# Kernel optimization log

Hardware: AMD Instinct MI355X
Metric: run time of the kernel (lower is better)

Reference implementation:

```python
import jax, jax.numpy as jnp
import numpy as np

D_MODEL = 256; N_HEADS = 8; N_LEVELS = 4; N_POINTS = 4
D_HEAD = D_MODEL // N_HEADS


def setup_inputs() -> dict:
    key = jax.random.key(0)
    ks = jax.random.split(key, 8)
    N, Lq = 4, 4096
    shapes = np.array([4096, 2048, 1024, 512], dtype=np.int32)  # temporal lengths per level
    Len_in = int(shapes.sum())  # 7680
    start = np.concatenate([[0], np.cumsum(shapes)[:-1]]).astype(np.int32)
    HLP = N_HEADS * N_LEVELS * N_POINTS
    return {
        "query": jax.random.normal(ks[0], (N, Lq, D_MODEL), jnp.float32),
        "reference_points": jax.random.uniform(ks[1], (N, Lq, N_LEVELS, 1), jnp.float32),
        "input_flatten": jax.random.normal(ks[2], (N, Len_in, D_MODEL), jnp.float32),
        "input_spatial_shapes": jnp.asarray(shapes),
        "input_level_start_index": jnp.asarray(start),
        "W_off": jax.random.normal(ks[3], (D_MODEL, HLP), jnp.float32) * 0.01,
        "b_off": jax.random.normal(ks[4], (HLP,), jnp.float32) * 2.0,
        "W_aw": jax.random.normal(ks[5], (D_MODEL, HLP), jnp.float32) * 0.02,
        "b_aw": jnp.zeros((HLP,), jnp.float32),
        "W_v": jax.random.normal(ks[6], (D_MODEL, D_MODEL), jnp.float32) / np.sqrt(D_MODEL).astype(np.float32),
        "b_v": jnp.zeros((D_MODEL,), jnp.float32),
        "W_out": jax.random.normal(ks[7], (D_MODEL, D_MODEL), jnp.float32) / np.sqrt(D_MODEL).astype(np.float32),
        "b_out": jnp.zeros((D_MODEL,), jnp.float32),
    }


def reference(query, reference_points, input_flatten, input_spatial_shapes,
              input_level_start_index, W_off, b_off, W_aw, b_aw, W_v, b_v,
              W_out, b_out):
    N, Lq, C = query.shape
    M, L, P, Dh = N_HEADS, N_LEVELS, N_POINTS, D_HEAD
    S = input_flatten.shape[1]

    value = (input_flatten @ W_v + b_v).reshape(N, S, M, Dh)
    off = (query @ W_off + b_off).reshape(N, Lq, M, L, P)
    aw = jax.nn.softmax((query @ W_aw + b_aw).reshape(N, Lq, M, L * P), axis=-1)
    aw = aw.reshape(N, Lq, M, L, P)

    # reference_points last dim == 1 branch: loc = ref + off / T_l, in [0,1]
    T = input_spatial_shapes.astype(jnp.float32)[None, None, None, :, None]  # [1,1,1,L,1]
    loc = reference_points[:, :, None, :, None, 0] + off / T  # [N,Lq,M,L,P]

    # grid_sample(align_corners=False, padding_mode='border') along W with H=1, y=0.5:
    # pixel coord x = loc*T - 0.5, clamped to [0, T-1], then linear interp.
    x = jnp.clip(loc * T - 0.5, 0.0, T - 1.0)
    x0 = jnp.floor(x)
    w1 = x - x0                                   # frac weight for right neighbor
    i0 = x0.astype(jnp.int32)
    i1 = jnp.minimum(i0 + 1, input_spatial_shapes[None, None, None, :, None] - 1)
    base = input_level_start_index[None, None, None, :, None]
    g0 = i0 + base                                # global flattened indices [N,Lq,M,L,P]
    g1 = i1 + base

    v = value.transpose(0, 2, 1, 3)               # [N,M,S,Dh]

    def gather(idx):
        idxt = idx.transpose(0, 2, 1, 3, 4).reshape(N, M, Lq * L * P, 1)
        return jnp.take_along_axis(v, idxt, axis=2).reshape(N, M, Lq, L, P, Dh)

    s0 = gather(g0)
    s1 = gather(g1)
    w1t = w1.transpose(0, 2, 1, 3, 4)[..., None]   # [N,M,Lq,L,P,1]
    samp = s0 * (1.0 - w1t) + s1 * w1t             # [N,M,Lq,L,P,Dh]

    awt = aw.transpose(0, 2, 1, 3, 4)[..., None]
    out = (samp * awt).sum(axis=(3, 4))            # [N,M,Lq,Dh]
    out = out.transpose(0, 2, 1, 3).reshape(N, Lq, M * Dh)
    return out @ W_out + b_out
```

## Files before the change

kernel.cpp:

```cpp
#include <hip/hip_runtime.h>
#include <hip/hip_bf16.h>
#include <cstddef>
#include <cstdint>

#define D_MODEL   256
#define N_HEADS   8
#define N_LEVELS  4
#define N_POINTS  4
#define D_HEAD    32
#define HLP       128
#define NBATCH    4
#define LQ        4096
#define S_LEN     7680

typedef __attribute__((ext_vector_type(8))) short  short8;
typedef __attribute__((ext_vector_type(4))) float  f32x4;
typedef __attribute__((ext_vector_type(4))) int    i32x4;
typedef __attribute__((ext_vector_type(8))) unsigned short ushort8;

__device__ __forceinline__ unsigned short f2bf(float x) {
    __hip_bfloat16 h = __float2bfloat16(x);
    return *reinterpret_cast<unsigned short*>(&h);
}
__device__ __forceinline__ float bf2f(unsigned short u) {
    unsigned int v = ((unsigned int)u) << 16;
    return *reinterpret_cast<float*>(&v);
}

__device__ __forceinline__ void gload_lds16(const void* g, void* l) {
    __builtin_amdgcn_global_load_lds(
        (const __attribute__((address_space(1))) void*)g,
        (__attribute__((address_space(3))) void*)l,
        16, 0, 0);
}

__global__ __launch_bounds__(256) void prep_kernel(
    const float* __restrict__ W_v,  const float* __restrict__ W_off,
    const float* __restrict__ W_aw, const float* __restrict__ W_out,
    const float* __restrict__ b_off, const float* __restrict__ b_aw,
    unsigned short* __restrict__ Wv_t, unsigned short* __restrict__ Wcat_t,
    unsigned short* __restrict__ Wout_t, float* __restrict__ bcat)
{
    __shared__ float t[64][65];
    const int z   = blockIdx.z;
    const int k0  = blockIdx.y * 64;
    const int n0  = blockIdx.x * 64;
    const int tid = threadIdx.x;

    const float* src; int srcN; int cs; unsigned short* dst;
    if (z == 0)      { src = W_v;   srcN = 256; cs = n0;       dst = Wv_t;  }
    else if (z == 2) { src = W_out; srcN = 256; cs = n0;       dst = Wout_t;}
    else if (n0 < 128){ src = W_off; srcN = 128; cs = n0;      dst = Wcat_t;}
    else             { src = W_aw;  srcN = 128; cs = n0 - 128; dst = Wcat_t;}

    #pragma unroll
    for (int i = 0; i < 16; ++i) {
        int idx = tid + i * 256;
        int kk = idx >> 6, nn = idx & 63;
        t[kk][nn] = src[(size_t)(k0 + kk) * srcN + cs + nn];
    }
    __syncthreads();
    #pragma unroll
    for (int i = 0; i < 16; ++i) {
        int idx = tid + i * 256;
        int nn = idx >> 6, kk = idx & 63;
        dst[(size_t)(n0 + nn) * 256 + k0 + kk] = f2bf(t[kk][nn]);
    }
    if (z == 1 && blockIdx.x == 0 && blockIdx.y == 0) {
        bcat[tid] = (tid < 128) ? b_off[tid] : b_aw[tid - 128];
    }
}

__global__ __launch_bounds__(256) void gemm_vp_kernel(
    const float* __restrict__ inflat, const float* __restrict__ query,
    const unsigned short* __restrict__ Wv_t, const unsigned short* __restrict__ Wcat_t,
    const float* __restrict__ b_v, const float* __restrict__ bcat,
    unsigned short* __restrict__ value3, float* __restrict__ P)
{
    __shared__ alignas(16) unsigned short Abuf[2][4][64][8];
    __shared__ alignas(16) unsigned short Bbuf[2][8][64][8];

    const int job = blockIdx.x;
    const bool is_val = (job < 960);
    const int jj   = is_val ? job : (job - 960);
    const int row0 = (jj >> 1) * 64;
    const int col0 = (jj & 1) * 128;
    const float* A = is_val ? inflat : query;
    const unsigned short* Bt = is_val ? Wv_t : Wcat_t;
    const float* bias = is_val ? b_v : bcat;

    const int tid  = threadIdx.x;
    const int lane = tid & 63;
    const int w    = tid >> 6;
    const int lr   = lane & 15;
    const int lk   = (lane >> 4) * 8;

    const int ar = tid >> 2;
    const int ak = (tid & 3) * 8;
    const int afrag = ar >> 4;
    const int alane = ((ak >> 3) << 4) | (ar & 15);
    const float* Arow = A + (size_t)(row0 + ar) * 256 + ak;
    const unsigned short* Bcol = Bt + (size_t)(col0 + lr) * 256 + lk;

    f32x4 acc[8] = {};

    float4 pa0 = *(const float4*)(Arow);
    float4 pa1 = *(const float4*)(Arow + 4);
    #pragma unroll
    for (int c = 0; c < 2; ++c) {
        const int in = w * 2 + c;
        gload_lds16(Bcol + (size_t)in * 16 * 256, &Bbuf[0][in][0][0]);
    }

    for (int kt = 0; kt < 8; ++kt) {
        const int cur = kt & 1;
        short8 pk;
        pk[0] = (short)f2bf(pa0.x); pk[1] = (short)f2bf(pa0.y);
        pk[2] = (short)f2bf(pa0.z); pk[3] = (short)f2bf(pa0.w);
        pk[4] = (short)f2bf(pa1.x); pk[5] = (short)f2bf(pa1.y);
        pk[6] = (short)f2bf(pa1.z); pk[7] = (short)f2bf(pa1.w);
        *(short8*)&Abuf[cur][afrag][alane][0] = pk;
        __syncthreads();

        if (kt < 7) {
            const int k1 = (kt + 1) * 32;
            pa0 = *(const float4*)(Arow + k1);
            pa1 = *(const float4*)(Arow + k1 + 4);
            #pragma unroll
            for (int c = 0; c < 2; ++c) {
                const int in = w * 2 + c;
                gload_lds16(Bcol + (size_t)in * 16 * 256 + k1, &Bbuf[1 - cur][in][0][0]);
            }
        }

        const short8 af = *(const short8*)&Abuf[cur][w][lane][0];
        #pragma unroll
        for (int j = 0; j < 8; ++j) {
            const short8 bf = *(const short8*)&Bbuf[cur][j][lane][0];
            acc[j] = __builtin_amdgcn_mfma_f32_16x16x32_bf16(af, bf, acc[j], 0, 0, 0);
        }
    }

    const int prow = (lane >> 4) * 4;
    const int pcol = lane & 15;
    const int rbase = row0 + w * 16 + prow;
    if (is_val) {
        const int n  = row0 / S_LEN;
        const int s0 = row0 - n * S_LEN + w * 16 + prow;
        #pragma unroll
        for (int j = 0; j < 8; ++j) {
            const int col = col0 + j * 16 + pcol;
            const float bs = bias[col];
            const int m = col >> 5, d = col & 31;
            unsigned short* dst = value3 + ((size_t)(n * 8 + m) * S_LEN + s0) * 32 + d;
            #pragma unroll
            for (int r = 0; r < 4; ++r)
                dst[(size_t)r * 32] = f2bf(acc[j][r] + bs);
        }
    } else {
        #pragma unroll
        for (int j = 0; j < 8; ++j) {
            const int col = col0 + j * 16 + pcol;
            const float bs = bias[col];
            #pragma unroll
            for (int r = 0; r < 4; ++r)
                P[(size_t)(rbase + r) * 256 + col] = acc[j][r] + bs;
        }
    }
}

__global__ __launch_bounds__(256) void sample_out_kernel(
    const float* __restrict__ P, const float* __restrict__ refp,
    const int* __restrict__ shapes, const int* __restrict__ lstart,
    const unsigned short* __restrict__ value3,
    const unsigned short* __restrict__ Wout_t,
    const float* __restrict__ b_out,
    float* __restrict__ Cout)
{
    __shared__ int   sG0[16][132];
    __shared__ float sW [16][132];
    __shared__ float sA [16][132];
    __shared__ alignas(16) unsigned short t_lds[16][264];
    __shared__ int   glim[4];

    const int b    = blockIdx.x;
    const int xcd  = b & 7;
    const int n    = xcd >> 1;
    const int half = xcd & 1;
    const int slot = b >> 3;
    const int q0   = (slot * 2 + half) * 16;
    const int nq0  = n * LQ + q0;
    const int tid  = threadIdx.x;

    if (tid < 4) glim[tid] = lstart[tid] + shapes[tid] - 1;

    #pragma unroll
    for (int it = 0; it < 2; ++it) {
        const int idx = tid + it * 256;
        const int q   = idx >> 5;
        const int sub = idx & 31;
        const int m   = sub >> 2;
        const int l   = sub & 3;
        const int j0  = m * 16 + l * 4;
        const int nq  = nq0 + q;
        const f32x4 off   = __builtin_nontemporal_load(
            (const f32x4*)(P + (size_t)nq * 256 + j0));
        const f32x4 logit = __builtin_nontemporal_load(
            (const f32x4*)(P + (size_t)nq * 256 + 128 + j0));
        const float ref   = refp[(size_t)nq * N_LEVELS + l];
        const int   sh    = shapes[l];
        const int   ls    = lstart[l];
        const float Tf    = (float)sh;
        i32x4 g4; f32x4 w4;
        #pragma unroll
        for (int k = 0; k < 4; ++k) {
            float x = ref * Tf + off[k] - 0.5f;
            x = fminf(fmaxf(x, 0.0f), Tf - 1.0f);
            const float x0 = floorf(x);
            g4[k] = (int)x0 + ls;
            w4[k] = x - x0;
        }
        *(i32x4*)&sG0[q][j0] = g4;
        *(f32x4*)&sW [q][j0] = w4;
        *(f32x4*)&sA [q][j0] = logit;
    }
    __syncthreads();

    #pragma unroll
    for (int it = 0; it < 2; ++it) {
        const int idx = tid + it * 256;
        const int q   = idx >> 5;
        const int sub = idx & 31;
        const int m   = sub >> 2;
        const int ql  = sub & 3;
        const unsigned short* vb =
            value3 + (size_t)(n * 8 + m) * S_LEN * 32 + ql * 8;

        float e[16];
        {
            const f32x4 a0 = *(const f32x4*)&sA[q][m * 16 + 0];
            const f32x4 a1 = *(const f32x4*)&sA[q][m * 16 + 4];
            const f32x4 a2 = *(const f32x4*)&sA[q][m * 16 + 8];
            const f32x4 a3 = *(const f32x4*)&sA[q][m * 16 + 12];
            #pragma unroll
            for (int k = 0; k < 4; ++k) {
                e[k] = a0[k]; e[4+k] = a1[k]; e[8+k] = a2[k]; e[12+k] = a3[k];
            }
        }
        float mx = -1e30f;
        #pragma unroll
        for (int i = 0; i < 16; ++i) mx = fmaxf(mx, e[i]);
        float s = 0.f;
        #pragma unroll
        for (int i = 0; i < 16; ++i) { e[i] = __expf(e[i] - mx); s += e[i]; }
        const float rs = 1.0f / s;

        float acc[8] = {};
        #pragma unroll
        for (int i = 0; i < 16; ++i) {
            const int j = m * 16 + i;
            const float a  = e[i] * rs;
            const float ww = sW[q][j];
            const int g0 = sG0[q][j];
            const int g1 = min(g0 + 1, glim[i >> 2]);
            const ushort8 u0 = *(const ushort8*)(vb + (size_t)g0 * 32);
            const ushort8 u1 = *(const ushort8*)(vb + (size_t)g1 * 32);
            #pragma unroll
            for (int d = 0; d < 8; ++d) {
                const float v0 = bf2f(u0[d]);
                const float v1 = bf2f(u1[d]);
                acc[d] += a * (v0 + ww * (v1 - v0));
            }
        }
        ushort8 o;
        #pragma unroll
        for (int d = 0; d < 8; ++d) o[d] = f2bf(acc[d]);
        *(ushort8*)&t_lds[q][m * 32 + ql * 8] = o;
    }
    __syncthreads();

    const int lane = tid & 63;
    const int wv   = tid >> 6;
    const int arow = lane & 15;
    const int kgrp = (lane >> 4) * 8;
    const int n0   = wv * 64;

    short8 af[8];
    #pragma unroll
    for (int kt = 0; kt < 8; ++kt)
        af[kt] = *(const short8*)&t_lds[arow][kt * 32 + kgrp];

    f32x4 oacc[4] = {};
    #pragma unroll
    for (int j = 0; j < 4; ++j) {
        const unsigned short* bp =
            Wout_t + (size_t)(n0 + j * 16 + arow) * 256 + kgrp;
        #pragma unroll
        for (int kt = 0; kt < 8; ++kt) {
            const short8 bf = *(const short8*)(bp + kt * 32);
            oacc[j] = __builtin_amdgcn_mfma_f32_16x16x32_bf16(af[kt], bf, oacc[j], 0, 0, 0);
        }
    }

    const int prow = (lane >> 4) * 4;
    const int pcol = lane & 15;
    #pragma unroll
    for (int j = 0; j < 4; ++j) {
        const int col = n0 + j * 16 + pcol;
        const float bs = b_out[col];
        #pragma unroll
        for (int r = 0; r < 4; ++r)
            __builtin_nontemporal_store(oacc[j][r] + bs,
                Cout + (size_t)(nq0 + prow + r) * 256 + col);
    }
}

extern "C" void kernel_launch(void* const* d_in, const int* in_sizes, int n_in,
                              void* d_out, int out_size, void* d_ws, size_t ws_size,
                              hipStream_t stream)
{
    const float* query  = (const float*)d_in[0];
    const float* refp   = (const float*)d_in[1];
    const float* inflat = (const float*)d_in[2];
    const int*   shapes = (const int*)d_in[3];
    const int*   lstart = (const int*)d_in[4];
    const float* W_off  = (const float*)d_in[5];
    const float* b_off  = (const float*)d_in[6];
    const float* W_aw   = (const float*)d_in[7];
    const float* b_aw   = (const float*)d_in[8];
    const float* W_v    = (const float*)d_in[9];
    const float* b_v    = (const float*)d_in[10];
    const float* W_out  = (const float*)d_in[11];
    const float* b_out  = (const float*)d_in[12];

    const int M_val = NBATCH * S_LEN;
    const int M_q   = NBATCH * LQ;

    char* p = (char*)d_ws;
    unsigned short* value3 = (unsigned short*)p; p += (size_t)M_val * D_MODEL * 2;
    float*          P      = (float*)p;          p += (size_t)M_q * 256 * 4;
    unsigned short* Wv_t   = (unsigned short*)p; p += 256 * 256 * 2;
    unsigned short* Wcat_t = (unsigned short*)p; p += 256 * 256 * 2;
    unsigned short* Wout_t = (unsigned short*)p; p += 256 * 256 * 2;
    float*          bcat   = (float*)p;          p += 256 * 4;

    prep_kernel<<<dim3(4, 4, 3), 256, 0, stream>>>(
        W_v, W_off, W_aw, W_out, b_off, b_aw, Wv_t, Wcat_t, Wout_t, bcat);
    gemm_vp_kernel<<<1472, 256, 0, stream>>>(
        inflat, query, Wv_t, Wcat_t, b_v, bcat, value3, P);
    sample_out_kernel<<<1024, 256, 0, stream>>>(
        P, refp, shapes, lstart, value3, Wout_t, b_out, (float*)d_out);
}
```

Before: 162.3 us.

## Use 512 threads per sample block and compute sampling params in registers

The sampling kernel now runs 512 threads per block, one thread per (query, head, quarter-dim) item, where before 256 threads each looped twice. Each thread computes its own sample indices, interpolation weights and softmax directly from P into registers, which drops the shared staging arrays and one block barrier. The output GEMM is split across 8 waves with 32 columns each. This adds parallelism and cuts LDS traffic, but each thread now loads redundant offset and logit data (four threads per head read the same values) and register pressure goes up.

```diff
diff --git a/kernel.cpp b/kernel.cpp
--- a/kernel.cpp
+++ b/kernel.cpp
@@ -169,7 +169,7 @@
     }
 }
 
-__global__ __launch_bounds__(256) void sample_out_kernel(
+__global__ __launch_bounds__(512, 4) void sample_out_kernel(
     const float* __restrict__ P, const float* __restrict__ refp,
     const int* __restrict__ shapes, const int* __restrict__ lstart,
     const unsigned short* __restrict__ value3,
@@ -177,11 +177,7 @@
     const float* __restrict__ b_out,
     float* __restrict__ Cout)
 {
-    __shared__ int   sG0[16][132];
-    __shared__ float sW [16][132];
-    __shared__ float sA [16][132];
     __shared__ alignas(16) unsigned short t_lds[16][264];
-    __shared__ int   glim[4];
 
     const int b    = blockIdx.x;
     const int xcd  = b & 7;
@@ -192,76 +188,55 @@
     const int nq0  = n * LQ + q0;
     const int tid  = threadIdx.x;
 
-    if (tid < 4) glim[tid] = lstart[tid] + shapes[tid] - 1;
-
-    #pragma unroll
-    for (int it = 0; it < 2; ++it) {
-        const int idx = tid + it * 256;
-        const int q   = idx >> 5;
-        const int sub = idx & 31;
-        const int m   = sub >> 2;
-        const int l   = sub & 3;
-        const int j0  = m * 16 + l * 4;
-        const int nq  = nq0 + q;
-        const f32x4 off   = __builtin_nontemporal_load(
-            (const f32x4*)(P + (size_t)nq * 256 + j0));
-        const f32x4 logit = __builtin_nontemporal_load(
-            (const f32x4*)(P + (size_t)nq * 256 + 128 + j0));
-        const float ref   = refp[(size_t)nq * N_LEVELS + l];
-        const int   sh    = shapes[l];
-        const int   ls    = lstart[l];
-        const float Tf    = (float)sh;
-        i32x4 g4; f32x4 w4;
-        #pragma unroll
-        for (int k = 0; k < 4; ++k) {
-            float x = ref * Tf + off[k] - 0.5f;
-            x = fminf(fmaxf(x, 0.0f), Tf - 1.0f);
-            const float x0 = floorf(x);
-            g4[k] = (int)x0 + ls;
-            w4[k] = x - x0;
-        }
-        *(i32x4*)&sG0[q][j0] = g4;
-        *(f32x4*)&sW [q][j0] = w4;
-        *(f32x4*)&sA [q][j0] = logit;
-    }
-    __syncthreads();
-
-    #pragma unroll
-    for (int it = 0; it < 2; ++it) {
-        const int idx = tid + it * 256;
-        const int q   = idx >> 5;
-        const int sub = idx & 31;
+    {
+        const int q   = tid >> 5;
+        const int sub = tid & 31;
         const int m   = sub >> 2;
         const int ql  = sub & 3;
+        const int nq  = nq0 + q;
+
+        const i32x4 sh4 = *(const i32x4*)shapes;
+        const i32x4 ls4 = *(const i32x4*)lstart;
+        const f32x4 rf4 = *(const f32x4*)(refp + (size_t)nq * N_LEVELS);
+
+        float e[16], wgt[16];
+        int   g0a[16], glim[4];
+        #pragma unroll
+        for (int l = 0; l < 4; ++l) {
+            const f32x4 off = __builtin_nontemporal_load(
+                (const f32x4*)(P + (size_t)nq * 256 + m * 16 + l * 4));
+            const f32x4 lg  = __builtin_nontemporal_load(
+                (const f32x4*)(P + (size_t)nq * 256 + 128 + m * 16 + l * 4));
+            const float Tf = (float)sh4[l];
+            glim[l] = ls4[l] + sh4[l] - 1;
+            #pragma unroll
+            for (int k = 0; k < 4; ++k) {
+                float x = rf4[l] * Tf + off[k] - 0.5f;
+                x = fminf(fmaxf(x, 0.0f), Tf - 1.0f);
+                const float x0 = floorf(x);
+                g0a[l * 4 + k] = (int)x0 + ls4[l];
+                wgt[l * 4 + k] = x - x0;
+                e  [l * 4 + k] = lg[k];
+            }
+        }
+
+        float mx = -1e30f;
+        #pragma unroll
+        for (int i = 0; i < 16; ++i) mx = fmaxf(mx, e[i]);
+        float s = 0.f;
+        #pragma unroll
+        for (int i = 0; i < 16; ++i) { e[i] = __expf(e[i] - mx); s += e[i]; }
+        const float rs = 1.0f / s;
+
         const unsigned short* vb =
             value3 + (size_t)(n * 8 + m) * S_LEN * 32 + ql * 8;
 
-        float e[16];
-        {
-            const f32x4 a0 = *(const f32x4*)&sA[q][m * 16 + 0];
-            const f32x4 a1 = *(const f32x4*)&sA[q][m * 16 + 4];
-            const f32x4 a2 = *(const f32x4*)&sA[q][m * 16 + 8];
-            const f32x4 a3 = *(const f32x4*)&sA[q][m * 16 + 12];
-            #pragma unroll
-            for (int k = 0; k < 4; ++k) {
-                e[k] = a0[k]; e[4+k] = a1[k]; e[8+k] = a2[k]; e[12+k] = a3[k];
-            }
-        }
-        float mx = -1e30f;
-        #pragma unroll
-        for (int i = 0; i < 16; ++i) mx = fmaxf(mx, e[i]);
-        float s = 0.f;
-        #pragma unroll
-        for (int i = 0; i < 16; ++i) { e[i] = __expf(e[i] - mx); s += e[i]; }
-        const float rs = 1.0f / s;
-
         float acc[8] = {};
         #pragma unroll
         for (int i = 0; i < 16; ++i) {
-            const int j = m * 16 + i;
             const float a  = e[i] * rs;
-            const float ww = sW[q][j];
-            const int g0 = sG0[q][j];
+            const float ww = wgt[i];
+            const int g0 = g0a[i];
             const int g1 = min(g0 + 1, glim[i >> 2]);
             const ushort8 u0 = *(const ushort8*)(vb + (size_t)g0 * 32);
             const ushort8 u1 = *(const ushort8*)(vb + (size_t)g1 * 32);
@@ -283,16 +258,16 @@
     const int wv   = tid >> 6;
     const int arow = lane & 15;
     const int kgrp = (lane >> 4) * 8;
-    const int n0   = wv * 64;
+    const int n0   = wv * 32;
 
     short8 af[8];
     #pragma unroll
     for (int kt = 0; kt < 8; ++kt)
         af[kt] = *(const short8*)&t_lds[arow][kt * 32 + kgrp];
 
-    f32x4 oacc[4] = {};
-    #pragma unroll
-    for (int j = 0; j < 4; ++j) {
+    f32x4 oacc[2] = {};
+    #pragma unroll
+    for (int j = 0; j < 2; ++j) {
         const unsigned short* bp =
             Wout_t + (size_t)(n0 + j * 16 + arow) * 256 + kgrp;
         #pragma unroll
@@ -305,7 +280,7 @@
     const int prow = (lane >> 4) * 4;
     const int pcol = lane & 15;
     #pragma unroll
-    for (int j = 0; j < 4; ++j) {
+    for (int j = 0; j < 2; ++j) {
         const int col = n0 + j * 16 + pcol;
         const float bs = b_out[col];
         #pragma unroll
@@ -348,6 +323,6 @@
         W_v, W_off, W_aw, W_out, b_off, b_aw, Wv_t, Wcat_t, Wout_t, bcat);
     gemm_vp_kernel<<<1472, 256, 0, stream>>>(
         inflat, query, Wv_t, Wcat_t, b_v, bcat, value3, P);
-    sample_out_kernel<<<1024, 256, 0, stream>>>(
+    sample_out_kernel<<<1024, 512, 0, stream>>>(
         P, refp, shapes, lstart, value3, Wout_t, b_out, (float*)d_out);
 }
```

Measured after the change: 168.5 us. 3.8% more time.
